# Optimization experiments

Measured on AMD Instinct MI355X. Metric: run time of the kernel, lower is better.

## Reference

```python
import jax, jax.numpy as jnp
import numpy as np


def setup_inputs() -> dict:
    key = jax.random.key(0)
    ks = jax.random.split(key, 20)
    B, T, m, p = 2048, 64, 128, 128
    L = 64
    sc = 0.1
    return {
        "hidden_states": jax.random.normal(ks[0], (B, T, m), jnp.float32),
        "y": jax.random.normal(ks[1], (B, L), jnp.float32),
        "FC1_w": jax.random.normal(ks[2], (m, 2 * p + m), jnp.float32) * sc,
        "FC1_b": jax.random.normal(ks[3], (m,), jnp.float32) * sc,
        "FC2_w": jax.random.normal(ks[4], (1, m), jnp.float32) * sc,
        "FC2_b": jax.random.normal(ks[5], (1,), jnp.float32) * sc,
        "FCin_w": jax.random.normal(ks[6], (1, m + 1), jnp.float32) * sc,
        "FCin_b": jax.random.normal(ks[7], (1,), jnp.float32) * sc,
        "W_ih": jax.random.normal(ks[8], (4 * p, 1), jnp.float32) * sc,
        "W_hh": jax.random.normal(ks[9], (4 * p, p), jnp.float32) * sc,
        "b_ih": jax.random.normal(ks[10], (4 * p,), jnp.float32) * sc,
        "b_hh": jax.random.normal(ks[11], (4 * p,), jnp.float32) * sc,
        "FCout1_w": jax.random.normal(ks[12], (p, p + m), jnp.float32) * sc,
        "FCout1_b": jax.random.normal(ks[13], (p,), jnp.float32) * sc,
        "FCout2_w": jax.random.normal(ks[14], (1, p), jnp.float32) * sc,
        "FCout2_b": jax.random.normal(ks[15], (1,), jnp.float32) * sc,
        "target_length": 64,
    }


def reference(hidden_states, y, FC1_w, FC1_b, FC2_w, FC2_b, FCin_w, FCin_b,
              W_ih, W_hh, b_ih, b_hh, FCout1_w, FCout1_b, FCout2_w, FCout2_b,
              target_length):
    B, T, m = hidden_states.shape
    p = W_hh.shape[1]

    def step(carry, y_t):
        d, s = carry  # (B,p) each
        # Temporal attention: concat([d, s, H]) over T, two-layer MLP, softmax over T
        dE = jnp.broadcast_to(d[:, None, :], (B, T, p))
        sE = jnp.broadcast_to(s[:, None, :], (B, T, p))
        h_concat = jnp.concatenate([dE, sE, hidden_states], axis=2)  # (B,T,2p+m)
        z = jnp.tanh(jnp.einsum('btk,mk->btm', h_concat, FC1_w) + FC1_b)
        logits = jnp.einsum('btm,om->bto', z, FC2_w) + FC2_b  # (B,T,1)
        alpha = jax.nn.softmax(logits, axis=1)
        C = jnp.sum(hidden_states * alpha, axis=1)  # (B,m)
        # FCin on [y_t, C]
        y_concat = jnp.concatenate([y_t[:, None], C], axis=1)  # (B,m+1)
        lstm_in = y_concat @ FCin_w.T + FCin_b  # (B,1)
        # torch LSTMCell: gates order i, f, g, o
        gates = lstm_in @ W_ih.T + b_ih + d @ W_hh.T + b_hh  # (B,4p)
        i, f, g, o = jnp.split(gates, 4, axis=1)
        s_new = jax.nn.sigmoid(f) * s + jax.nn.sigmoid(i) * jnp.tanh(g)
        d_new = jax.nn.sigmoid(o) * jnp.tanh(s_new)
        # output MLP (ELU despite the name ReLU in source)
        fc_in = jnp.concatenate([d_new, C], axis=1)  # (B,p+m)
        h = jax.nn.elu(fc_in @ FCout1_w.T + FCout1_b)
        out = (h @ FCout2_w.T + FCout2_b)[:, 0]  # (B,)
        return (d_new, s_new), out

    d0 = jnp.zeros((B, p), hidden_states.dtype)
    s0 = jnp.zeros((B, p), hidden_states.dtype)
    y_ts = jnp.swapaxes(y[:, :target_length], 0, 1)  # (L,B)
    _, outs = jax.lax.scan(step, (d0, s0), y_ts)
    return jnp.swapaxes(outs, 0, 1)  # (B, target_length)
```

## Files before the change

kernel.cpp:

```cpp
#include <hip/hip_runtime.h>
#include <hip/hip_bf16.h>

typedef short bf16x8 __attribute__((ext_vector_type(8)));
typedef float f32x4 __attribute__((ext_vector_type(4)));

#define LOG2E 1.4426950408889634f

__device__ __forceinline__ float fexp(float x){ return __builtin_amdgcn_exp2f(x * LOG2E); }
__device__ __forceinline__ float frcp(float x){ return __builtin_amdgcn_rcpf(x); }
__device__ __forceinline__ float tanh_fast(float x){ float e = fexp(2.f*x); return 1.f - 2.f*frcp(e + 1.f); }
__device__ __forceinline__ float sigm_fast(float x){ return frcp(1.f + fexp(-x)); }
__device__ __forceinline__ float elu_fast(float x){ return x > 0.f ? x : fexp(x) - 1.f; }
__device__ __forceinline__ float dot4(float4 a, float4 b){
  return (a.x*b.x + a.y*b.y) + (a.z*b.z + a.w*b.w);
}
__device__ __forceinline__ float wsum(float v){
  #pragma unroll
  for (int o = 32; o > 0; o >>= 1) v += __shfl_xor(v, o, 64);
  return v;
}
__device__ __forceinline__ unsigned pk2(float a, float b){
  unsigned lo = __bfloat16_as_ushort(__float2bfloat16(a));
  unsigned hi = __bfloat16_as_ushort(__float2bfloat16(b));
  return lo | (hi << 16);
}
__device__ __forceinline__ float bflo(unsigned u){ return __uint_as_float(u << 16); }
__device__ __forceinline__ float bfhi(unsigned u){ return __uint_as_float(u & 0xffff0000u); }

__device__ __forceinline__ int afrag_off(int kt, int lanep){
  int off = (kt << 10) + (lanep << 4);
  off ^= ((lanep >> 4) & 1) << 5;
  off ^= (kt & 1) << 6;
  return off;
}

__global__ void k_prep(const float* __restrict__ FC1_w, const float* __restrict__ W_hh,
                       const float* __restrict__ FCout1_w,
                       const float* __restrict__ b_ih, const float* __restrict__ b_hh,
                       unsigned short* __restrict__ B1f, unsigned short* __restrict__ B2f,
                       unsigned short* __restrict__ B3f, float* __restrict__ bio)
{
  int n = blockIdx.x * 256 + threadIdx.x;
  if (n < 32768) {
    int jj = n & 7, lane = (n >> 3) & 63, ktn = n >> 9;
    int kt = ktn & 7, nt = ktn >> 3;
    int nn = nt*16 + (lane & 15), k = kt*32 + ((lane >> 4) << 3) + jj;
    B1f[n] = __bfloat16_as_ushort(__float2bfloat16(FC1_w[nn*384 + k]));
  } else if (n < 98304) {
    int n2 = n - 32768;
    int jj = n2 & 7, lane = (n2 >> 3) & 63, ktn = n2 >> 9;
    int kt = ktn & 3, nt = ktn >> 2;
    int nn = nt*16 + (lane & 15), k = kt*32 + ((lane >> 4) << 3) + jj;
    B2f[n2] = __bfloat16_as_ushort(__float2bfloat16(W_hh[nn*128 + k]));
  } else if (n < 131072) {
    int n3 = n - 98304;
    int jj = n3 & 7, lane = (n3 >> 3) & 63, ktn = n3 >> 9;
    int kt = ktn & 7, nt = ktn >> 3;
    int nn = nt*16 + (lane & 15), k = kt*32 + ((lane >> 4) << 3) + jj;
    B3f[n3] = __bfloat16_as_ushort(__float2bfloat16(FCout1_w[nn*256 + k]));
  } else if (n < 131584) {
    int n4 = n - 131072;
    bio[n4] = b_ih[n4] + b_hh[n4];
  }
}

__global__ __launch_bounds__(256) void k_hw(
    const float* __restrict__ H, const float* __restrict__ FC1_w,
    const float* __restrict__ FC1_b, unsigned short* __restrict__ HWp,
    unsigned short* __restrict__ Hbf)
{
  __shared__ __align__(16) float Hl[64][128];
  const int b = blockIdx.x, tid = threadIdx.x;
  const float* Hb = H + (size_t)b * 8192;
  for (int i = tid; i < 8192; i += 256) ((float*)Hl)[i] = Hb[i];
  __syncthreads();

  if (Hbf) {
    unsigned* Ho = (unsigned*)Hbf + (size_t)b * 4096;
    for (int i = tid; i < 4096; i += 256) {
      float2 v = ((const float2*)Hl)[i];
      Ho[i] = pk2(v.x, v.y);
    }
  }

  const int m = tid >> 1, t0 = (tid & 1) * 32;
  float acc[32];
  const float bias = FC1_b[m];
  #pragma unroll
  for (int j = 0; j < 32; ++j) acc[j] = bias;

  const float* wrow = FC1_w + m*384 + 256;
  for (int k4 = 0; k4 < 32; ++k4) {
    float4 w = *(const float4*)(wrow + 4*k4);
    #pragma unroll
    for (int j = 0; j < 32; ++j) {
      float4 h = *(const float4*)&Hl[t0 + j][4*k4];
      acc[j] += dot4(w, h);
    }
  }
  unsigned short* o = HWp + (((size_t)b*32 + (m >> 2))*64 + t0)*4 + (m & 3);
  #pragma unroll
  for (int j = 0; j < 32; ++j)
    o[j*4] = __bfloat16_as_ushort(__float2bfloat16(acc[j]));
}

template<bool HB>
__global__ __launch_bounds__(512, 2) void k_main(
    const float* __restrict__ H, const float* __restrict__ Y,
    const unsigned short* __restrict__ HWp, const unsigned short* __restrict__ Hbf,
    const unsigned short* __restrict__ B1f, const unsigned short* __restrict__ B2f,
    const unsigned short* __restrict__ B3f, const float* __restrict__ bio,
    const float* __restrict__ FC2_w, const float* __restrict__ FCin_w,
    const float* __restrict__ FCin_b, const float* __restrict__ W_ih,
    const float* __restrict__ FCout1_b, const float* __restrict__ FCout2_w,
    const float* __restrict__ FCout2_b, float* __restrict__ out, int L)
{
  __shared__ __align__(16) char  AFds[8192];
  __shared__ __align__(16) char  AFdc[8192];
  __shared__ __align__(16) float a_l[8][128];
  __shared__ __align__(16) float ho_l[8][128];
  __shared__ __align__(16) float gate_l[8][512];
  __shared__ __align__(16) float alpha_l[8][64];
  __shared__ __align__(16) float fc2s[128], fo2s[128], fo1bs[128], fcinC[128];
  __shared__ __align__(16) float bios[512], wihs[512];
  __shared__ float scal[4];

  const int tid = threadIdx.x, w = tid >> 6, lane = tid & 63;

  if (tid < 128) {
    fc2s[tid] = FC2_w[tid]; fo2s[tid] = FCout2_w[tid];
    fo1bs[tid] = FCout1_b[tid]; fcinC[tid] = FCin_w[1 + tid];
  }
  bios[tid] = bio[tid];
  wihs[tid] = W_ih[tid];
  if (tid == 0) { scal[0] = FCin_b[0]; scal[1] = FCout2_b[0]; scal[2] = FCin_w[0]; }
  #pragma unroll
  for (int i = 0; i < 4; ++i) {
    ((int*)AFds)[tid*4 + i] = 0;
    ((int*)AFdc)[tid*4 + i] = 0;
  }
  __syncthreads();

  const bf16x8* B1v = (const bf16x8*)B1f;
  const bf16x8* B2v = (const bf16x8*)B2f;
  const bf16x8* B3v = (const bf16x8*)B3f;
  bf16x8 wA[8], wG[4][4], wO[8];
  #pragma unroll
  for (int kt = 0; kt < 8; ++kt) wA[kt] = B1v[(w*8 + kt)*64 + lane];
  #pragma unroll
  for (int t2 = 0; t2 < 4; ++t2)
    #pragma unroll
    for (int kt = 0; kt < 4; ++kt) wG[t2][kt] = B2v[((w*4 + t2)*4 + kt)*64 + lane];
  #pragma unroll
  for (int kt = 0; kt < 8; ++kt) wO[kt] = B3v[(w*8 + kt)*64 + lane];

  const int b = blockIdx.x * 8 + w;
  const uint2* HWu = (const uint2*)HWp + (size_t)b * 2048;
  const unsigned* Hbu = (const unsigned*)Hbf + (size_t)b * 4096;
  const float2* Hf2 = (const float2*)(H + (size_t)b * 8192);

  float2 sst = {0.f, 0.f};
  const int drow = (lane >> 4) * 4;
  const bool dvalid = (lane < 32);
  const int ncb = lane & 15;
  const int j = lane << 1;

  for (int step = 0; step < L; ++step) {
    bf16x8 af[8];
    #pragma unroll
    for (int kt = 0; kt < 8; ++kt) af[kt] = *(const bf16x8*)&AFds[afrag_off(kt, lane)];
    f32x4 accA = {0.f,0.f,0.f,0.f};
    #pragma unroll
    for (int kt = 0; kt < 8; ++kt)
      accA = __builtin_amdgcn_mfma_f32_16x16x32_bf16(af[kt], wA[kt], accA, 0, 0, 0);
    f32x4 aG[4];
    #pragma unroll
    for (int t2 = 0; t2 < 4; ++t2) {
      f32x4 acc = {0.f,0.f,0.f,0.f};
      #pragma unroll
      for (int kt = 0; kt < 4; ++kt)
        acc = __builtin_amdgcn_mfma_f32_16x16x32_bf16(af[kt], wG[t2][kt], acc, 0, 0, 0);
      aG[t2] = acc;
    }
    if (dvalid) {
      int nc = w*16 + ncb;
      #pragma unroll
      for (int r2 = 0; r2 < 4; ++r2) a_l[drow + r2][nc] = accA[r2];
      #pragma unroll
      for (int t2 = 0; t2 < 4; ++t2) {
        int ng = (w*4 + t2)*16 + ncb;
        #pragma unroll
        for (int r2 = 0; r2 < 4; ++r2) gate_l[drow + r2][ng] = aG[t2][r2];
      }
    }
    __syncthreads();

    float lg = 0.f;
    #pragma unroll 4
    for (int m4 = 0; m4 < 32; ++m4) {
      uint2 u = HWu[m4*64 + lane];
      float4 av = *(const float4*)&a_l[w][m4*4];
      float4 fv = *(const float4*)&fc2s[m4*4];
      lg += fv.x * tanh_fast(av.x + bflo(u.x));
      lg += fv.y * tanh_fast(av.y + bfhi(u.x));
      lg += fv.z * tanh_fast(av.z + bflo(u.y));
      lg += fv.w * tanh_fast(av.w + bfhi(u.y));
    }
    float ex = fexp(lg);
    float alpha = ex * frcp(wsum(ex));
    alpha_l[w][lane] = alpha;

    float cx = 0.f, cy = 0.f;
    #pragma unroll 4
    for (int t4 = 0; t4 < 16; ++t4) {
      float4 av = *(const float4*)&alpha_l[w][t4*4];
      if (HB) {
        unsigned h0 = Hbu[(t4*4 + 0)*64 + lane];
        unsigned h1 = Hbu[(t4*4 + 1)*64 + lane];
        unsigned h2 = Hbu[(t4*4 + 2)*64 + lane];
        unsigned h3 = Hbu[(t4*4 + 3)*64 + lane];
        cx += av.x*bflo(h0); cy += av.x*bfhi(h0);
        cx += av.y*bflo(h1); cy += av.y*bfhi(h1);
        cx += av.z*bflo(h2); cy += av.z*bfhi(h2);
        cx += av.w*bflo(h3); cy += av.w*bfhi(h3);
      } else {
        float2 h0 = Hf2[(t4*4 + 0)*64 + lane];
        float2 h1 = Hf2[(t4*4 + 1)*64 + lane];
        float2 h2 = Hf2[(t4*4 + 2)*64 + lane];
        float2 h3 = Hf2[(t4*4 + 3)*64 + lane];
        cx += av.x*h0.x; cy += av.x*h0.y;
        cx += av.y*h1.x; cy += av.y*h1.y;
        cx += av.z*h2.x; cy += av.z*h2.y;
        cx += av.w*h3.x; cy += av.w*h3.y;
      }
    }

    float2 fcv = *(const float2*)&fcinC[j];
    float part = wsum(fcv.x*cx + fcv.y*cy);
    float yt = Y[(size_t)b*64 + step];
    float li = part + scal[2]*yt + scal[0];

    float2 gi = *(const float2*)&gate_l[w][j];
    float2 gf = *(const float2*)&gate_l[w][128 + j];
    float2 gg = *(const float2*)&gate_l[w][256 + j];
    float2 go = *(const float2*)&gate_l[w][384 + j];
    float2 wv, bv;
    wv = *(const float2*)&wihs[j];       bv = *(const float2*)&bios[j];
    gi.x += li*wv.x + bv.x; gi.y += li*wv.y + bv.y;
    wv = *(const float2*)&wihs[128 + j]; bv = *(const float2*)&bios[128 + j];
    gf.x += li*wv.x + bv.x; gf.y += li*wv.y + bv.y;
    wv = *(const float2*)&wihs[256 + j]; bv = *(const float2*)&bios[256 + j];
    gg.x += li*wv.x + bv.x; gg.y += li*wv.y + bv.y;
    wv = *(const float2*)&wihs[384 + j]; bv = *(const float2*)&bios[384 + j];
    go.x += li*wv.x + bv.x; go.y += li*wv.y + bv.y;

    sst.x = sigm_fast(gf.x)*sst.x + sigm_fast(gi.x)*tanh_fast(gg.x);
    sst.y = sigm_fast(gf.y)*sst.y + sigm_fast(gi.y)*tanh_fast(gg.y);
    float dx = sigm_fast(go.x)*tanh_fast(sst.x);
    float dy = sigm_fast(go.y)*tanh_fast(sst.y);

    unsigned dp = pk2(dx, dy), sp = pk2(sst.x, sst.y), cp = pk2(cx, cy);
    {
      int kt0 = j >> 5, g0 = (j >> 3) & 3, bo = (j & 7) * 2;
      int k1 = 128 + j, kt1 = k1 >> 5, g1 = (k1 >> 3) & 3;
      *(unsigned*)&AFds[afrag_off(kt0, w + 16*g0) + bo] = dp;
      *(unsigned*)&AFdc[afrag_off(kt0, w + 16*g0) + bo] = dp;
      *(unsigned*)&AFds[afrag_off(kt1, w + 16*g1) + bo] = sp;
      *(unsigned*)&AFdc[afrag_off(kt1, w + 16*g1) + bo] = cp;
    }
    __syncthreads();

    f32x4 accO = {0.f,0.f,0.f,0.f};
    #pragma unroll
    for (int kt = 0; kt < 8; ++kt) {
      bf16x8 afc = *(const bf16x8*)&AFdc[afrag_off(kt, lane)];
      accO = __builtin_amdgcn_mfma_f32_16x16x32_bf16(afc, wO[kt], accO, 0, 0, 0);
    }
    if (dvalid) {
      int nc = w*16 + ncb;
      #pragma unroll
      for (int r2 = 0; r2 < 4; ++r2) ho_l[drow + r2][nc] = accO[r2];
    }
    __syncthreads();

    float2 hv = *(const float2*)&ho_l[w][j];
    float2 bb = *(const float2*)&fo1bs[j];
    float e0 = elu_fast(hv.x + bb.x), e1 = elu_fast(hv.y + bb.y);
    float2 fv2 = *(const float2*)&fo2s[j];
    float op = wsum(fv2.x*e0 + fv2.y*e1);
    if (lane == 0) out[(size_t)b*L + step] = op + scal[1];
  }
}

extern "C" void kernel_launch(void* const* d_in, const int* in_sizes, int n_in,
                              void* d_out, int out_size, void* d_ws, size_t ws_size,
                              hipStream_t stream) {
  const float* H        = (const float*)d_in[0];
  const float* y        = (const float*)d_in[1];
  const float* FC1_w    = (const float*)d_in[2];
  const float* FC1_b    = (const float*)d_in[3];
  const float* FC2_w    = (const float*)d_in[4];
  const float* FCin_w   = (const float*)d_in[6];
  const float* FCin_b   = (const float*)d_in[7];
  const float* W_ih     = (const float*)d_in[8];
  const float* W_hh     = (const float*)d_in[9];
  const float* b_ih     = (const float*)d_in[10];
  const float* b_hh     = (const float*)d_in[11];
  const float* FCout1_w = (const float*)d_in[12];
  const float* FCout1_b = (const float*)d_in[13];
  const float* FCout2_w = (const float*)d_in[14];
  const float* FCout2_b = (const float*)d_in[15];
  float* out = (float*)d_out;
  const int L = out_size / 2048;

  char* ws = (char*)d_ws;
  unsigned short* B1f = (unsigned short*)(ws + 0);
  unsigned short* B2f = (unsigned short*)(ws + 65536);
  unsigned short* B3f = (unsigned short*)(ws + 196608);
  float*          bio = (float*)(ws + 262144);
  unsigned short* HWp = (unsigned short*)(ws + 264192);
  unsigned short* Hbf = (unsigned short*)(ws + 264192 + 33554432);
  const bool hb = ws_size >= (size_t)(264192 + 2*33554432);

  k_prep<<<514, 256, 0, stream>>>(FC1_w, W_hh, FCout1_w, b_ih, b_hh,
                                  B1f, B2f, B3f, bio);
  k_hw<<<2048, 256, 0, stream>>>(H, FC1_w, FC1_b, HWp, hb ? Hbf : nullptr);
  if (hb)
    k_main<true><<<256, 512, 0, stream>>>(H, y, HWp, Hbf, B1f, B2f, B3f, bio,
                                          FC2_w, FCin_w, FCin_b, W_ih,
                                          FCout1_b, FCout2_w, FCout2_b, out, L);
  else
    k_main<false><<<256, 512, 0, stream>>>(H, y, HWp, Hbf, B1f, B2f, B3f, bio,
                                           FC2_w, FCin_w, FCin_b, W_ih,
                                           FCout1_b, FCout2_w, FCout2_b, out, L);
}
```

Before: 830.1 us.

## Split each batch row across two waves and defer output MLP to next step

Raises the main recurrent kernel from 512 to 1024 threads so two wavefronts share each batch row. They split the attention logit reduction over m and the context/LSTM elementwise work over p, and divide the MFMA work: one wave computes the attention projection, the other the output-MLP projection. The output MLP for step t is overlapped into step t+1, with a final epilogue for the last step. This doubles per-row parallelism on a latency-bound recurrence and removes one barrier-separated phase per step, at the cost of extra syncthreads for cross-wave reductions and lower register budget per thread (launch bounds 1024,4).

```diff
diff --git a/kernel.cpp b/kernel.cpp
--- a/kernel.cpp
+++ b/kernel.cpp
@@ -26,6 +26,9 @@
 }
 __device__ __forceinline__ float bflo(unsigned u){ return __uint_as_float(u << 16); }
 __device__ __forceinline__ float bfhi(unsigned u){ return __uint_as_float(u & 0xffff0000u); }
+__device__ __forceinline__ unsigned short bfq(float a){
+  return __bfloat16_as_ushort(__float2bfloat16(a));
+}
 
 __device__ __forceinline__ int afrag_off(int kt, int lanep){
   int off = (kt << 10) + (lanep << 4);
@@ -45,19 +48,19 @@
     int jj = n & 7, lane = (n >> 3) & 63, ktn = n >> 9;
     int kt = ktn & 7, nt = ktn >> 3;
     int nn = nt*16 + (lane & 15), k = kt*32 + ((lane >> 4) << 3) + jj;
-    B1f[n] = __bfloat16_as_ushort(__float2bfloat16(FC1_w[nn*384 + k]));
+    B1f[n] = bfq(FC1_w[nn*384 + k]);
   } else if (n < 98304) {
     int n2 = n - 32768;
     int jj = n2 & 7, lane = (n2 >> 3) & 63, ktn = n2 >> 9;
     int kt = ktn & 3, nt = ktn >> 2;
     int nn = nt*16 + (lane & 15), k = kt*32 + ((lane >> 4) << 3) + jj;
-    B2f[n2] = __bfloat16_as_ushort(__float2bfloat16(W_hh[nn*128 + k]));
+    B2f[n2] = bfq(W_hh[nn*128 + k]);
   } else if (n < 131072) {
     int n3 = n - 98304;
     int jj = n3 & 7, lane = (n3 >> 3) & 63, ktn = n3 >> 9;
     int kt = ktn & 7, nt = ktn >> 3;
     int nn = nt*16 + (lane & 15), k = kt*32 + ((lane >> 4) << 3) + jj;
-    B3f[n3] = __bfloat16_as_ushort(__float2bfloat16(FCout1_w[nn*256 + k]));
+    B3f[n3] = bfq(FCout1_w[nn*256 + k]);
   } else if (n < 131584) {
     int n4 = n - 131072;
     bio[n4] = b_ih[n4] + b_hh[n4];
@@ -101,11 +104,11 @@
   unsigned short* o = HWp + (((size_t)b*32 + (m >> 2))*64 + t0)*4 + (m & 3);
   #pragma unroll
   for (int j = 0; j < 32; ++j)
-    o[j*4] = __bfloat16_as_ushort(__float2bfloat16(acc[j]));
+    o[j*4] = bfq(acc[j]);
 }
 
 template<bool HB>
-__global__ __launch_bounds__(512, 2) void k_main(
+__global__ __launch_bounds__(1024, 4) void k_main(
     const float* __restrict__ H, const float* __restrict__ Y,
     const unsigned short* __restrict__ HWp, const unsigned short* __restrict__ Hbf,
     const unsigned short* __restrict__ B1f, const unsigned short* __restrict__ B2f,
@@ -120,176 +123,180 @@
   __shared__ __align__(16) float a_l[8][128];
   __shared__ __align__(16) float ho_l[8][128];
   __shared__ __align__(16) float gate_l[8][512];
-  __shared__ __align__(16) float alpha_l[8][64];
+  __shared__ __align__(16) float lgp[8][2][64];
+  __shared__ float redp[8][2], outp[8][2];
   __shared__ __align__(16) float fc2s[128], fo2s[128], fo1bs[128], fcinC[128];
   __shared__ __align__(16) float bios[512], wihs[512];
   __shared__ float scal[4];
 
   const int tid = threadIdx.x, w = tid >> 6, lane = tid & 63;
+  const int r = w >> 1, h = w & 1;
+  const int oi = h*64 + lane;
 
   if (tid < 128) {
     fc2s[tid] = FC2_w[tid]; fo2s[tid] = FCout2_w[tid];
     fo1bs[tid] = FCout1_b[tid]; fcinC[tid] = FCin_w[1 + tid];
   }
-  bios[tid] = bio[tid];
-  wihs[tid] = W_ih[tid];
+  if (tid >= 256 && tid < 768) { bios[tid-256] = bio[tid-256]; wihs[tid-256] = W_ih[tid-256]; }
   if (tid == 0) { scal[0] = FCin_b[0]; scal[1] = FCout2_b[0]; scal[2] = FCin_w[0]; }
-  #pragma unroll
-  for (int i = 0; i < 4; ++i) {
-    ((int*)AFds)[tid*4 + i] = 0;
-    ((int*)AFdc)[tid*4 + i] = 0;
-  }
+  ((int*)AFds)[tid*2] = 0; ((int*)AFds)[tid*2+1] = 0;
+  ((int*)AFdc)[tid*2] = 0; ((int*)AFdc)[tid*2+1] = 0;
   __syncthreads();
 
-  const bf16x8* B1v = (const bf16x8*)B1f;
+  const bf16x8* BUv = (const bf16x8*)(h ? B3f : B1f);
   const bf16x8* B2v = (const bf16x8*)B2f;
-  const bf16x8* B3v = (const bf16x8*)B3f;
-  bf16x8 wA[8], wG[4][4], wO[8];
-  #pragma unroll
-  for (int kt = 0; kt < 8; ++kt) wA[kt] = B1v[(w*8 + kt)*64 + lane];
-  #pragma unroll
-  for (int t2 = 0; t2 < 4; ++t2)
+  bf16x8 wAO[8], wG[2][4];
+  #pragma unroll
+  for (int kt = 0; kt < 8; ++kt) wAO[kt] = BUv[(r*8 + kt)*64 + lane];
+  #pragma unroll
+  for (int t2 = 0; t2 < 2; ++t2)
     #pragma unroll
-    for (int kt = 0; kt < 4; ++kt) wG[t2][kt] = B2v[((w*4 + t2)*4 + kt)*64 + lane];
-  #pragma unroll
-  for (int kt = 0; kt < 8; ++kt) wO[kt] = B3v[(w*8 + kt)*64 + lane];
-
-  const int b = blockIdx.x * 8 + w;
-  const uint2* HWu = (const uint2*)HWp + (size_t)b * 2048;
+    for (int kt = 0; kt < 4; ++kt) wG[t2][kt] = B2v[((w*2 + t2)*4 + kt)*64 + lane];
+
+  const int b = blockIdx.x * 8 + r;
+  const uint2* HWu = (const uint2*)HWp + (size_t)b * 2048 + (size_t)h * 1024;
   const unsigned* Hbu = (const unsigned*)Hbf + (size_t)b * 4096;
-  const float2* Hf2 = (const float2*)(H + (size_t)b * 8192);
-
-  float2 sst = {0.f, 0.f};
+  const float* Hf = H + (size_t)b * 8192;
+  const int hbase = h*32 + (lane >> 1);
+  const int shamt = (lane & 1) ? 0 : 16;
+
   const int drow = (lane >> 4) * 4;
   const bool dvalid = (lane < 32);
   const int ncb = lane & 15;
-  const int j = lane << 1;
+  const int p_kt = oi >> 5, p_g = (oi >> 3) & 3, p_bo = (oi & 7) * 2;
+  const int p_off = afrag_off(p_kt, r + 16*p_g) + p_bo;
+  const int p_off_s = afrag_off(4 + p_kt, r + 16*p_g) + p_bo;
+
+  float sst = 0.f;
 
   for (int step = 0; step < L; ++step) {
-    bf16x8 af[8];
-    #pragma unroll
-    for (int kt = 0; kt < 8; ++kt) af[kt] = *(const bf16x8*)&AFds[afrag_off(kt, lane)];
-    f32x4 accA = {0.f,0.f,0.f,0.f};
-    #pragma unroll
-    for (int kt = 0; kt < 8; ++kt)
-      accA = __builtin_amdgcn_mfma_f32_16x16x32_bf16(af[kt], wA[kt], accA, 0, 0, 0);
-    f32x4 aG[4];
-    #pragma unroll
-    for (int t2 = 0; t2 < 4; ++t2) {
-      f32x4 acc = {0.f,0.f,0.f,0.f};
-      #pragma unroll
-      for (int kt = 0; kt < 4; ++kt)
-        acc = __builtin_amdgcn_mfma_f32_16x16x32_bf16(af[kt], wG[t2][kt], acc, 0, 0, 0);
-      aG[t2] = acc;
+    f32x4 accU = {0.f,0.f,0.f,0.f};
+    f32x4 aG0 = {0.f,0.f,0.f,0.f}, aG1 = {0.f,0.f,0.f,0.f};
+    if (h == 0) {
+      bf16x8 af[8];
+      #pragma unroll
+      for (int kt = 0; kt < 8; ++kt) af[kt] = *(const bf16x8*)&AFds[afrag_off(kt, lane)];
+      #pragma unroll
+      for (int kt = 0; kt < 8; ++kt)
+        accU = __builtin_amdgcn_mfma_f32_16x16x32_bf16(af[kt], wAO[kt], accU, 0, 0, 0);
+      #pragma unroll
+      for (int kt = 0; kt < 4; ++kt) {
+        aG0 = __builtin_amdgcn_mfma_f32_16x16x32_bf16(af[kt], wG[0][kt], aG0, 0, 0, 0);
+        aG1 = __builtin_amdgcn_mfma_f32_16x16x32_bf16(af[kt], wG[1][kt], aG1, 0, 0, 0);
+      }
+    } else {
+      if (step > 0) {
+        #pragma unroll
+        for (int kt = 0; kt < 8; ++kt) {
+          bf16x8 afc = *(const bf16x8*)&AFdc[afrag_off(kt, lane)];
+          accU = __builtin_amdgcn_mfma_f32_16x16x32_bf16(afc, wAO[kt], accU, 0, 0, 0);
+        }
+      }
+      #pragma unroll
+      for (int kt = 0; kt < 4; ++kt) {
+        bf16x8 af2 = *(const bf16x8*)&AFds[afrag_off(kt, lane)];
+        aG0 = __builtin_amdgcn_mfma_f32_16x16x32_bf16(af2, wG[0][kt], aG0, 0, 0, 0);
+        aG1 = __builtin_amdgcn_mfma_f32_16x16x32_bf16(af2, wG[1][kt], aG1, 0, 0, 0);
+      }
     }
     if (dvalid) {
-      int nc = w*16 + ncb;
-      #pragma unroll
-      for (int r2 = 0; r2 < 4; ++r2) a_l[drow + r2][nc] = accA[r2];
-      #pragma unroll
-      for (int t2 = 0; t2 < 4; ++t2) {
-        int ng = (w*4 + t2)*16 + ncb;
+      if (h == 0) {
         #pragma unroll
-        for (int r2 = 0; r2 < 4; ++r2) gate_l[drow + r2][ng] = aG[t2][r2];
+        for (int r2 = 0; r2 < 4; ++r2) a_l[drow + r2][r*16 + ncb] = accU[r2];
+      } else if (step > 0) {
+        #pragma unroll
+        for (int r2 = 0; r2 < 4; ++r2) ho_l[drow + r2][r*16 + ncb] = accU[r2];
+      }
+      #pragma unroll
+      for (int r2 = 0; r2 < 4; ++r2) {
+        gate_l[drow + r2][(w*2)*16 + ncb]     = aG0[r2];
+        gate_l[drow + r2][(w*2 + 1)*16 + ncb] = aG1[r2];
       }
     }
     __syncthreads();
 
-    float lg = 0.f;
+    if (step > 0) {
+      float e = elu_fast(ho_l[r][oi] + fo1bs[oi]);
+      float op = wsum(fo2s[oi] * e);
+      if (lane == 0) outp[r][h] = op;
+    }
+
+    float lg0 = 0.f, lg1 = 0.f, lg2 = 0.f, lg3 = 0.f;
     #pragma unroll 4
-    for (int m4 = 0; m4 < 32; ++m4) {
+    for (int m4 = 0; m4 < 16; ++m4) {
       uint2 u = HWu[m4*64 + lane];
-      float4 av = *(const float4*)&a_l[w][m4*4];
-      float4 fv = *(const float4*)&fc2s[m4*4];
-      lg += fv.x * tanh_fast(av.x + bflo(u.x));
-      lg += fv.y * tanh_fast(av.y + bfhi(u.x));
-      lg += fv.z * tanh_fast(av.z + bflo(u.y));
-      lg += fv.w * tanh_fast(av.w + bfhi(u.y));
-    }
-    float ex = fexp(lg);
+      float4 av = *(const float4*)&a_l[r][h*64 + m4*4];
+      float4 fv = *(const float4*)&fc2s[h*64 + m4*4];
+      lg0 += fv.x * tanh_fast(av.x + bflo(u.x));
+      lg1 += fv.y * tanh_fast(av.y + bfhi(u.x));
+      lg2 += fv.z * tanh_fast(av.z + bflo(u.y));
+      lg3 += fv.w * tanh_fast(av.w + bfhi(u.y));
+    }
+    lgp[r][h][lane] = (lg0 + lg1) + (lg2 + lg3);
+    __syncthreads();
+
+    if (step > 0 && h == 0 && lane == 0)
+      out[(size_t)b*L + step - 1] = outp[r][0] + outp[r][1] + scal[1];
+
+    float lgt = lgp[r][0][lane] + lgp[r][1][lane];
+    float ex = fexp(lgt);
     float alpha = ex * frcp(wsum(ex));
-    alpha_l[w][lane] = alpha;
-
-    float cx = 0.f, cy = 0.f;
-    #pragma unroll 4
-    for (int t4 = 0; t4 < 16; ++t4) {
-      float4 av = *(const float4*)&alpha_l[w][t4*4];
+
+    float c = 0.f;
+    #pragma unroll 8
+    for (int t = 0; t < 64; ++t) {
+      float at = __shfl(alpha, t);
       if (HB) {
-        unsigned h0 = Hbu[(t4*4 + 0)*64 + lane];
-        unsigned h1 = Hbu[(t4*4 + 1)*64 + lane];
-        unsigned h2 = Hbu[(t4*4 + 2)*64 + lane];
-        unsigned h3 = Hbu[(t4*4 + 3)*64 + lane];
-        cx += av.x*bflo(h0); cy += av.x*bfhi(h0);
-        cx += av.y*bflo(h1); cy += av.y*bfhi(h1);
-        cx += av.z*bflo(h2); cy += av.z*bfhi(h2);
-        cx += av.w*bflo(h3); cy += av.w*bfhi(h3);
+        unsigned u = Hbu[t*64 + hbase];
+        c += at * __uint_as_float((u << shamt) & 0xffff0000u);
       } else {
-        float2 h0 = Hf2[(t4*4 + 0)*64 + lane];
-        float2 h1 = Hf2[(t4*4 + 1)*64 + lane];
-        float2 h2 = Hf2[(t4*4 + 2)*64 + lane];
-        float2 h3 = Hf2[(t4*4 + 3)*64 + lane];
-        cx += av.x*h0.x; cy += av.x*h0.y;
-        cx += av.y*h1.x; cy += av.y*h1.y;
-        cx += av.z*h2.x; cy += av.z*h2.y;
-        cx += av.w*h3.x; cy += av.w*h3.y;
-      }
-    }
-
-    float2 fcv = *(const float2*)&fcinC[j];
-    float part = wsum(fcv.x*cx + fcv.y*cy);
+        c += at * Hf[t*128 + oi];
+      }
+    }
+    float part = wsum(fcinC[oi] * c);
+    if (lane == 0) redp[r][h] = part;
+    __syncthreads();
+
     float yt = Y[(size_t)b*64 + step];
-    float li = part + scal[2]*yt + scal[0];
-
-    float2 gi = *(const float2*)&gate_l[w][j];
-    float2 gf = *(const float2*)&gate_l[w][128 + j];
-    float2 gg = *(const float2*)&gate_l[w][256 + j];
-    float2 go = *(const float2*)&gate_l[w][384 + j];
-    float2 wv, bv;
-    wv = *(const float2*)&wihs[j];       bv = *(const float2*)&bios[j];
-    gi.x += li*wv.x + bv.x; gi.y += li*wv.y + bv.y;
-    wv = *(const float2*)&wihs[128 + j]; bv = *(const float2*)&bios[128 + j];
-    gf.x += li*wv.x + bv.x; gf.y += li*wv.y + bv.y;
-    wv = *(const float2*)&wihs[256 + j]; bv = *(const float2*)&bios[256 + j];
-    gg.x += li*wv.x + bv.x; gg.y += li*wv.y + bv.y;
-    wv = *(const float2*)&wihs[384 + j]; bv = *(const float2*)&bios[384 + j];
-    go.x += li*wv.x + bv.x; go.y += li*wv.y + bv.y;
-
-    sst.x = sigm_fast(gf.x)*sst.x + sigm_fast(gi.x)*tanh_fast(gg.x);
-    sst.y = sigm_fast(gf.y)*sst.y + sigm_fast(gi.y)*tanh_fast(gg.y);
-    float dx = sigm_fast(go.x)*tanh_fast(sst.x);
-    float dy = sigm_fast(go.y)*tanh_fast(sst.y);
-
-    unsigned dp = pk2(dx, dy), sp = pk2(sst.x, sst.y), cp = pk2(cx, cy);
-    {
-      int kt0 = j >> 5, g0 = (j >> 3) & 3, bo = (j & 7) * 2;
-      int k1 = 128 + j, kt1 = k1 >> 5, g1 = (k1 >> 3) & 3;
-      *(unsigned*)&AFds[afrag_off(kt0, w + 16*g0) + bo] = dp;
-      *(unsigned*)&AFdc[afrag_off(kt0, w + 16*g0) + bo] = dp;
-      *(unsigned*)&AFds[afrag_off(kt1, w + 16*g1) + bo] = sp;
-      *(unsigned*)&AFdc[afrag_off(kt1, w + 16*g1) + bo] = cp;
-    }
+    float li = redp[r][0] + redp[r][1] + scal[2]*yt + scal[0];
+
+    float gi = gate_l[r][      oi] + li*wihs[      oi] + bios[      oi];
+    float gf = gate_l[r][128 + oi] + li*wihs[128 + oi] + bios[128 + oi];
+    float gg = gate_l[r][256 + oi] + li*wihs[256 + oi] + bios[256 + oi];
+    float go = gate_l[r][384 + oi] + li*wihs[384 + oi] + bios[384 + oi];
+
+    sst = sigm_fast(gf)*sst + sigm_fast(gi)*tanh_fast(gg);
+    float dn = sigm_fast(go)*tanh_fast(sst);
+
+    unsigned short dq = bfq(dn), sq = bfq(sst), cq = bfq(c);
+    *(unsigned short*)&AFds[p_off]   = dq;
+    *(unsigned short*)&AFdc[p_off]   = dq;
+    *(unsigned short*)&AFds[p_off_s] = sq;
+    *(unsigned short*)&AFdc[p_off_s] = cq;
     __syncthreads();
-
+  }
+
+  if (h == 1) {
     f32x4 accO = {0.f,0.f,0.f,0.f};
     #pragma unroll
     for (int kt = 0; kt < 8; ++kt) {
       bf16x8 afc = *(const bf16x8*)&AFdc[afrag_off(kt, lane)];
-      accO = __builtin_amdgcn_mfma_f32_16x16x32_bf16(afc, wO[kt], accO, 0, 0, 0);
+      accO = __builtin_amdgcn_mfma_f32_16x16x32_bf16(afc, wAO[kt], accO, 0, 0, 0);
     }
     if (dvalid) {
-      int nc = w*16 + ncb;
-      #pragma unroll
-      for (int r2 = 0; r2 < 4; ++r2) ho_l[drow + r2][nc] = accO[r2];
-    }
-    __syncthreads();
-
-    float2 hv = *(const float2*)&ho_l[w][j];
-    float2 bb = *(const float2*)&fo1bs[j];
-    float e0 = elu_fast(hv.x + bb.x), e1 = elu_fast(hv.y + bb.y);
-    float2 fv2 = *(const float2*)&fo2s[j];
-    float op = wsum(fv2.x*e0 + fv2.y*e1);
-    if (lane == 0) out[(size_t)b*L + step] = op + scal[1];
-  }
+      #pragma unroll
+      for (int r2 = 0; r2 < 4; ++r2) ho_l[drow + r2][r*16 + ncb] = accO[r2];
+    }
+  }
+  __syncthreads();
+  {
+    float e = elu_fast(ho_l[r][oi] + fo1bs[oi]);
+    float op = wsum(fo2s[oi] * e);
+    if (lane == 0) outp[r][h] = op;
+  }
+  __syncthreads();
+  if (h == 0 && lane == 0)
+    out[(size_t)b*L + L - 1] = outp[r][0] + outp[r][1] + scal[1];
 }
 
 extern "C" void kernel_launch(void* const* d_in, const int* in_sizes, int n_in,
@@ -326,11 +333,11 @@
                                   B1f, B2f, B3f, bio);
   k_hw<<<2048, 256, 0, stream>>>(H, FC1_w, FC1_b, HWp, hb ? Hbf : nullptr);
   if (hb)
-    k_main<true><<<256, 512, 0, stream>>>(H, y, HWp, Hbf, B1f, B2f, B3f, bio,
-                                          FC2_w, FCin_w, FCin_b, W_ih,
-                                          FCout1_b, FCout2_w, FCout2_b, out, L);
-  else
-    k_main<false><<<256, 512, 0, stream>>>(H, y, HWp, Hbf, B1f, B2f, B3f, bio,
+    k_main<true><<<256, 1024, 0, stream>>>(H, y, HWp, Hbf, B1f, B2f, B3f, bio,
                                            FC2_w, FCin_w, FCin_b, W_ih,
                                            FCout1_b, FCout2_w, FCout2_b, out, L);
-}
+  else
+    k_main<false><<<256, 1024, 0, stream>>>(H, y, HWp, Hbf, B1f, B2f, B3f, bio,
+                                            FC2_w, FCin_w, FCin_b, W_ih,
+                                            FCout1_b, FCout2_w, FCout2_b, out, L);
+}
```

Result: slower. 2.121 ms (+155.5%).

## Precompute H·FCin per timestep and defer output MLP to next step

Applied to the files above, without the earlier changes.

Precomputes P[b,t] = H[b,t,:]·FCin_w[1:] in the prep kernel, so the LSTM input becomes a softmax-weighted sum of P. This takes the context vector C off the critical path of the gate update, and C is now only needed for the output MLP. The output-layer MFMAs for step s-1 are merged into step s's first MFMA phase, which removes one __syncthreads and one LDS phase per step; the final step is handled after the loop. Y is also staged in LDS. In exchange, k_hw does a bit more work and the workspace layout shifts.

```diff
diff --git a/kernel.cpp b/kernel.cpp
--- a/kernel.cpp
+++ b/kernel.cpp
@@ -26,6 +26,9 @@
 }
 __device__ __forceinline__ float bflo(unsigned u){ return __uint_as_float(u << 16); }
 __device__ __forceinline__ float bfhi(unsigned u){ return __uint_as_float(u & 0xffff0000u); }
+__device__ __forceinline__ unsigned short bfq(float a){
+  return __bfloat16_as_ushort(__float2bfloat16(a));
+}
 
 __device__ __forceinline__ int afrag_off(int kt, int lanep){
   int off = (kt << 10) + (lanep << 4);
@@ -45,19 +48,19 @@
     int jj = n & 7, lane = (n >> 3) & 63, ktn = n >> 9;
     int kt = ktn & 7, nt = ktn >> 3;
     int nn = nt*16 + (lane & 15), k = kt*32 + ((lane >> 4) << 3) + jj;
-    B1f[n] = __bfloat16_as_ushort(__float2bfloat16(FC1_w[nn*384 + k]));
+    B1f[n] = bfq(FC1_w[nn*384 + k]);
   } else if (n < 98304) {
     int n2 = n - 32768;
     int jj = n2 & 7, lane = (n2 >> 3) & 63, ktn = n2 >> 9;
     int kt = ktn & 3, nt = ktn >> 2;
     int nn = nt*16 + (lane & 15), k = kt*32 + ((lane >> 4) << 3) + jj;
-    B2f[n2] = __bfloat16_as_ushort(__float2bfloat16(W_hh[nn*128 + k]));
+    B2f[n2] = bfq(W_hh[nn*128 + k]);
   } else if (n < 131072) {
     int n3 = n - 98304;
     int jj = n3 & 7, lane = (n3 >> 3) & 63, ktn = n3 >> 9;
     int kt = ktn & 7, nt = ktn >> 3;
     int nn = nt*16 + (lane & 15), k = kt*32 + ((lane >> 4) << 3) + jj;
-    B3f[n3] = __bfloat16_as_ushort(__float2bfloat16(FCout1_w[nn*256 + k]));
+    B3f[n3] = bfq(FCout1_w[nn*256 + k]);
   } else if (n < 131584) {
     int n4 = n - 131072;
     bio[n4] = b_ih[n4] + b_hh[n4];
@@ -66,7 +69,8 @@
 
 __global__ __launch_bounds__(256) void k_hw(
     const float* __restrict__ H, const float* __restrict__ FC1_w,
-    const float* __restrict__ FC1_b, unsigned short* __restrict__ HWp,
+    const float* __restrict__ FC1_b, const float* __restrict__ FCin_w,
+    unsigned short* __restrict__ HWp, float* __restrict__ P,
     unsigned short* __restrict__ Hbf)
 {
   __shared__ __align__(16) float Hl[64][128];
@@ -82,6 +86,16 @@
       Ho[i] = pk2(v.x, v.y);
     }
   }
+  if (tid < 64) {
+    float acc = 0.f;
+    #pragma unroll 8
+    for (int k4 = 0; k4 < 32; ++k4) {
+      float4 h = *(const float4*)&Hl[tid][4*k4];
+      float4 f = *(const float4*)&FCin_w[1 + 4*k4];
+      acc += dot4(h, f);
+    }
+    P[(size_t)b*64 + tid] = acc;
+  }
 
   const int m = tid >> 1, t0 = (tid & 1) * 32;
   float acc[32];
@@ -101,17 +115,18 @@
   unsigned short* o = HWp + (((size_t)b*32 + (m >> 2))*64 + t0)*4 + (m & 3);
   #pragma unroll
   for (int j = 0; j < 32; ++j)
-    o[j*4] = __bfloat16_as_ushort(__float2bfloat16(acc[j]));
+    o[j*4] = bfq(acc[j]);
 }
 
 template<bool HB>
 __global__ __launch_bounds__(512, 2) void k_main(
-    const float* __restrict__ H, const float* __restrict__ Y,
+    const float* __restrict__ Hf_, const float* __restrict__ Y,
     const unsigned short* __restrict__ HWp, const unsigned short* __restrict__ Hbf,
     const unsigned short* __restrict__ B1f, const unsigned short* __restrict__ B2f,
     const unsigned short* __restrict__ B3f, const float* __restrict__ bio,
-    const float* __restrict__ FC2_w, const float* __restrict__ FCin_w,
-    const float* __restrict__ FCin_b, const float* __restrict__ W_ih,
+    const float* __restrict__ FC2_w, const float* __restrict__ Pg,
+    const float* __restrict__ FCin_w, const float* __restrict__ FCin_b,
+    const float* __restrict__ W_ih,
     const float* __restrict__ FCout1_b, const float* __restrict__ FCout2_w,
     const float* __restrict__ FCout2_b, float* __restrict__ out, int L)
 {
@@ -121,7 +136,8 @@
   __shared__ __align__(16) float ho_l[8][128];
   __shared__ __align__(16) float gate_l[8][512];
   __shared__ __align__(16) float alpha_l[8][64];
-  __shared__ __align__(16) float fc2s[128], fo2s[128], fo1bs[128], fcinC[128];
+  __shared__ __align__(16) float y_l[8][64];
+  __shared__ __align__(16) float fc2s[128], fo2s[128], fo1bs[128];
   __shared__ __align__(16) float bios[512], wihs[512];
   __shared__ float scal[4];
 
@@ -129,10 +145,11 @@
 
   if (tid < 128) {
     fc2s[tid] = FC2_w[tid]; fo2s[tid] = FCout2_w[tid];
-    fo1bs[tid] = FCout1_b[tid]; fcinC[tid] = FCin_w[1 + tid];
+    fo1bs[tid] = FCout1_b[tid];
   }
   bios[tid] = bio[tid];
   wihs[tid] = W_ih[tid];
+  y_l[tid >> 6][tid & 63] = Y[((size_t)(blockIdx.x*8 + (tid >> 6)))*64 + (tid & 63)];
   if (tid == 0) { scal[0] = FCin_b[0]; scal[1] = FCout2_b[0]; scal[2] = FCin_w[0]; }
   #pragma unroll
   for (int i = 0; i < 4; ++i) {
@@ -157,22 +174,34 @@
   const int b = blockIdx.x * 8 + w;
   const uint2* HWu = (const uint2*)HWp + (size_t)b * 2048;
   const unsigned* Hbu = (const unsigned*)Hbf + (size_t)b * 4096;
-  const float2* Hf2 = (const float2*)(H + (size_t)b * 8192);
+  const float2* Hf2 = (const float2*)(Hf_ + (size_t)b * 8192);
+  const float pP = Pg[(size_t)b*64 + lane];
 
   float2 sst = {0.f, 0.f};
   const int drow = (lane >> 4) * 4;
   const bool dvalid = (lane < 32);
   const int ncb = lane & 15;
   const int j = lane << 1;
+  const int p_g = (j >> 3) & 3, p_bo = (j & 7) * 2;
+  const int p_off   = afrag_off(j >> 5,       w + 16*p_g) + p_bo;
+  const int p_off_s = afrag_off(4 + (j >> 5), w + 16*p_g) + p_bo;
 
   for (int step = 0; step < L; ++step) {
-    bf16x8 af[8];
+    bf16x8 af[8], ac[4];
     #pragma unroll
     for (int kt = 0; kt < 8; ++kt) af[kt] = *(const bf16x8*)&AFds[afrag_off(kt, lane)];
-    f32x4 accA = {0.f,0.f,0.f,0.f};
+    #pragma unroll
+    for (int kt = 0; kt < 4; ++kt) ac[kt] = *(const bf16x8*)&AFdc[afrag_off(4 + kt, lane)];
+
+    f32x4 accA = {0.f,0.f,0.f,0.f}, accO = {0.f,0.f,0.f,0.f};
     #pragma unroll
     for (int kt = 0; kt < 8; ++kt)
       accA = __builtin_amdgcn_mfma_f32_16x16x32_bf16(af[kt], wA[kt], accA, 0, 0, 0);
+    #pragma unroll
+    for (int kt = 0; kt < 4; ++kt) {
+      accO = __builtin_amdgcn_mfma_f32_16x16x32_bf16(af[kt], wO[kt], accO, 0, 0, 0);
+      accO = __builtin_amdgcn_mfma_f32_16x16x32_bf16(ac[kt], wO[4 + kt], accO, 0, 0, 0);
+    }
     f32x4 aG[4];
     #pragma unroll
     for (int t2 = 0; t2 < 4; ++t2) {
@@ -185,7 +214,10 @@
     if (dvalid) {
       int nc = w*16 + ncb;
       #pragma unroll
-      for (int r2 = 0; r2 < 4; ++r2) a_l[drow + r2][nc] = accA[r2];
+      for (int r2 = 0; r2 < 4; ++r2) {
+        a_l[drow + r2][nc]  = accA[r2];
+        ho_l[drow + r2][nc] = accO[r2];
+      }
       #pragma unroll
       for (int t2 = 0; t2 < 4; ++t2) {
         int ng = (w*4 + t2)*16 + ncb;
@@ -195,23 +227,61 @@
     }
     __syncthreads();
 
-    float lg = 0.f;
-    #pragma unroll 4
+    if (step > 0) {
+      float e0 = elu_fast(ho_l[w][lane]      + fo1bs[lane]);
+      float e1 = elu_fast(ho_l[w][lane + 64] + fo1bs[lane + 64]);
+      float op = wsum(fo2s[lane]*e0 + fo2s[lane + 64]*e1);
+      if (lane == 0) out[(size_t)b*L + step - 1] = op + scal[1];
+    }
+
+    float lg0 = 0.f, lg1 = 0.f;
+    #pragma unroll 8
     for (int m4 = 0; m4 < 32; ++m4) {
       uint2 u = HWu[m4*64 + lane];
       float4 av = *(const float4*)&a_l[w][m4*4];
       float4 fv = *(const float4*)&fc2s[m4*4];
-      lg += fv.x * tanh_fast(av.x + bflo(u.x));
-      lg += fv.y * tanh_fast(av.y + bfhi(u.x));
-      lg += fv.z * tanh_fast(av.z + bflo(u.y));
-      lg += fv.w * tanh_fast(av.w + bfhi(u.y));
-    }
+      lg0 += fv.x * tanh_fast(av.x + bflo(u.x));
+      lg1 += fv.y * tanh_fast(av.y + bfhi(u.x));
+      lg0 += fv.z * tanh_fast(av.z + bflo(u.y));
+      lg1 += fv.w * tanh_fast(av.w + bfhi(u.y));
+    }
+    float lg = lg0 + lg1;
+
     float ex = fexp(lg);
-    float alpha = ex * frcp(wsum(ex));
+    float se  = wsum(ex);
+    float sep = wsum(ex * pP);
+    float inv = frcp(se);
+    float alpha = ex * inv;
     alpha_l[w][lane] = alpha;
+    float yt = y_l[w][step];
+    float li = sep * inv + scal[2]*yt + scal[0];
+
+    float2 gi = *(const float2*)&gate_l[w][j];
+    float2 gf = *(const float2*)&gate_l[w][128 + j];
+    float2 gg = *(const float2*)&gate_l[w][256 + j];
+    float2 go = *(const float2*)&gate_l[w][384 + j];
+    float2 wv, bv;
+    wv = *(const float2*)&wihs[j];       bv = *(const float2*)&bios[j];
+    gi.x += li*wv.x + bv.x; gi.y += li*wv.y + bv.y;
+    wv = *(const float2*)&wihs[128 + j]; bv = *(const float2*)&bios[128 + j];
+    gf.x += li*wv.x + bv.x; gf.y += li*wv.y + bv.y;
+    wv = *(const float2*)&wihs[256 + j]; bv = *(const float2*)&bios[256 + j];
+    gg.x += li*wv.x + bv.x; gg.y += li*wv.y + bv.y;
+    wv = *(const float2*)&wihs[384 + j]; bv = *(const float2*)&bios[384 + j];
+    go.x += li*wv.x + bv.x; go.y += li*wv.y + bv.y;
+
+    sst.x = sigm_fast(gf.x)*sst.x + sigm_fast(gi.x)*tanh_fast(gg.x);
+    sst.y = sigm_fast(gf.y)*sst.y + sigm_fast(gi.y)*tanh_fast(gg.y);
+    float dx = sigm_fast(go.x)*tanh_fast(sst.x);
+    float dy = sigm_fast(go.y)*tanh_fast(sst.y);
+
+    unsigned dp = pk2(dx, dy), sp = pk2(sst.x, sst.y);
+    *(unsigned*)&AFds[p_off]   = dp;
+    *(unsigned*)&AFdc[p_off]   = dp;
+    *(unsigned*)&AFds[p_off_s] = sp;
 
     float cx = 0.f, cy = 0.f;
-    #pragma unroll 4
+    #pragma unroll 8
     for (int t4 = 0; t4 < 16; ++t4) {
       float4 av = *(const float4*)&alpha_l[w][t4*4];
       if (HB) {
@@ -234,61 +304,29 @@
         cx += av.w*h3.x; cy += av.w*h3.y;
       }
     }
-
-    float2 fcv = *(const float2*)&fcinC[j];
-    float part = wsum(fcv.x*cx + fcv.y*cy);
-    float yt = Y[(size_t)b*64 + step];
-    float li = part + scal[2]*yt + scal[0];
-
-    float2 gi = *(const float2*)&gate_l[w][j];
-    float2 gf = *(const float2*)&gate_l[w][128 + j];
-    float2 gg = *(const float2*)&gate_l[w][256 + j];
-    float2 go = *(const float2*)&gate_l[w][384 + j];
-    float2 wv, bv;
-    wv = *(const float2*)&wihs[j];       bv = *(const float2*)&bios[j];
-    gi.x += li*wv.x + bv.x; gi.y += li*wv.y + bv.y;
-    wv = *(const float2*)&wihs[128 + j]; bv = *(const float2*)&bios[128 + j];
-    gf.x += li*wv.x + bv.x; gf.y += li*wv.y + bv.y;
-    wv = *(const float2*)&wihs[256 + j]; bv = *(const float2*)&bios[256 + j];
-    gg.x += li*wv.x + bv.x; gg.y += li*wv.y + bv.y;
-    wv = *(const float2*)&wihs[384 + j]; bv = *(const float2*)&bios[384 + j];
-    go.x += li*wv.x + bv.x; go.y += li*wv.y + bv.y;
-
-    sst.x = sigm_fast(gf.x)*sst.x + sigm_fast(gi.x)*tanh_fast(gg.x);
-    sst.y = sigm_fast(gf.y)*sst.y + sigm_fast(gi.y)*tanh_fast(gg.y);
-    float dx = sigm_fast(go.x)*tanh_fast(sst.x);
-    float dy = sigm_fast(go.y)*tanh_fast(sst.y);
-
-    unsigned dp = pk2(dx, dy), sp = pk2(sst.x, sst.y), cp = pk2(cx, cy);
-    {
-      int kt0 = j >> 5, g0 = (j >> 3) & 3, bo = (j & 7) * 2;
-      int k1 = 128 + j, kt1 = k1 >> 5, g1 = (k1 >> 3) & 3;
-      *(unsigned*)&AFds[afrag_off(kt0, w + 16*g0) + bo] = dp;
-      *(unsigned*)&AFdc[afrag_off(kt0, w + 16*g0) + bo] = dp;
-      *(unsigned*)&AFds[afrag_off(kt1, w + 16*g1) + bo] = sp;
-      *(unsigned*)&AFdc[afrag_off(kt1, w + 16*g1) + bo] = cp;
-    }
+    *(unsigned*)&AFdc[p_off_s] = pk2(cx, cy);
     __syncthreads();
-
+  }
+
+  {
     f32x4 accO = {0.f,0.f,0.f,0.f};
     #pragma unroll
     for (int kt = 0; kt < 8; ++kt) {
-      bf16x8 afc = *(const bf16x8*)&AFdc[afrag_off(kt, lane)];
-      accO = __builtin_amdgcn_mfma_f32_16x16x32_bf16(afc, wO[kt], accO, 0, 0, 0);
+      bf16x8 a = *(const bf16x8*)&AFdc[afrag_off(kt, lane)];
+      accO = __builtin_amdgcn_mfma_f32_16x16x32_bf16(a, wO[kt], accO, 0, 0, 0);
     }
     if (dvalid) {
       int nc = w*16 + ncb;
       #pragma unroll
       for (int r2 = 0; r2 < 4; ++r2) ho_l[drow + r2][nc] = accO[r2];
     }
-    __syncthreads();
-
-    float2 hv = *(const float2*)&ho_l[w][j];
-    float2 bb = *(const float2*)&fo1bs[j];
-    float e0 = elu_fast(hv.x + bb.x), e1 = elu_fast(hv.y + bb.y);
-    float2 fv2 = *(const float2*)&fo2s[j];
-    float op = wsum(fv2.x*e0 + fv2.y*e1);
-    if (lane == 0) out[(size_t)b*L + step] = op + scal[1];
+  }
+  __syncthreads();
+  {
+    float e0 = elu_fast(ho_l[w][lane]      + fo1bs[lane]);
+    float e1 = elu_fast(ho_l[w][lane + 64] + fo1bs[lane + 64]);
+    float op = wsum(fo2s[lane]*e0 + fo2s[lane + 64]*e1);
+    if (lane == 0) out[(size_t)b*L + L - 1] = op + scal[1];
   }
 }
 
@@ -318,19 +356,21 @@
   unsigned short* B2f = (unsigned short*)(ws + 65536);
   unsigned short* B3f = (unsigned short*)(ws + 196608);
   float*          bio = (float*)(ws + 262144);
-  unsigned short* HWp = (unsigned short*)(ws + 264192);
-  unsigned short* Hbf = (unsigned short*)(ws + 264192 + 33554432);
-  const bool hb = ws_size >= (size_t)(264192 + 2*33554432);
+  float*          P   = (float*)(ws + 264192);
+  unsigned short* HWp = (unsigned short*)(ws + 788480);
+  unsigned short* Hbf = (unsigned short*)(ws + 788480 + 33554432);
+  const bool hb = ws_size >= (size_t)(788480 + 2*33554432);
 
   k_prep<<<514, 256, 0, stream>>>(FC1_w, W_hh, FCout1_w, b_ih, b_hh,
                                   B1f, B2f, B3f, bio);
-  k_hw<<<2048, 256, 0, stream>>>(H, FC1_w, FC1_b, HWp, hb ? Hbf : nullptr);
+  k_hw<<<2048, 256, 0, stream>>>(H, FC1_w, FC1_b, FCin_w, HWp, P,
+                                 hb ? Hbf : nullptr);
   if (hb)
     k_main<true><<<256, 512, 0, stream>>>(H, y, HWp, Hbf, B1f, B2f, B3f, bio,
-                                          FC2_w, FCin_w, FCin_b, W_ih,
+                                          FC2_w, P, FCin_w, FCin_b, W_ih,
                                           FCout1_b, FCout2_w, FCout2_b, out, L);
   else
     k_main<false><<<256, 512, 0, stream>>>(H, y, HWp, Hbf, B1f, B2f, B3f, bio,
-                                           FC2_w, FCin_w, FCin_b, W_ih,
+                                           FC2_w, P, FCin_w, FCin_b, W_ih,
                                            FCout1_b, FCout2_w, FCout2_b, out, L);
 }
```

Result: slower. 1.345 ms (+62.0%).
